# Kernel tuning notes

Hardware: AMD Instinct MI355X
Metric: run time of the kernel (lower is better)

The kernel has to match this reference:

```python
import jax, jax.numpy as jnp
import numpy as np

N = 100000   # nodes
E = 1600000  # edges (before self loops)
F = 64       # num_features
H = 64       # hidden_channels
C = 10       # num_classes
G = 128      # graphs in batch
NEG_SLOPE = 0.2


def setup_inputs() -> dict:
    key = jax.random.key(0)
    ks = jax.random.split(key, 16)
    x = jax.random.normal(ks[0], (N, F), dtype=jnp.float32)
    edge_index = jax.random.randint(ks[1], (2, E), 0, N, dtype=jnp.int64)
    batch = jnp.sort(jax.random.randint(ks[2], (N,), 0, G, dtype=jnp.int64))
    def glorot(k, shape):
        fan = shape[0] + shape[-1]
        return jax.random.uniform(k, shape, jnp.float32, -1.0, 1.0) * np.sqrt(6.0 / fan)
    return {
        "x": x, "edge_index": edge_index, "batch": batch,
        # GATConv 1 (F -> H)
        "W1": glorot(ks[3], (F, H)), "as1": glorot(ks[4], (H,)), "ad1": glorot(ks[5], (H,)), "b1": jnp.zeros((H,), jnp.float32),
        # GATConv 2 (H -> H)
        "W2": glorot(ks[6], (H, H)), "as2": glorot(ks[7], (H,)), "ad2": glorot(ks[8], (H,)), "b2": jnp.zeros((H,), jnp.float32),
        # MLP head
        "mw1": glorot(ks[9], (H, H)), "mb1": jnp.zeros((H,), jnp.float32),
        "mw2": glorot(ks[10], (H, C)), "mb2": jnp.zeros((C,), jnp.float32),
    }


def gat_conv(x, src, dst, W, a_s, a_d, b):
    # x: [N, Fin] -> h: [N, Fout]
    h = x @ W
    # per-node attention halves, gathered per edge (heads=1)
    al_s = h @ a_s   # [N]
    al_d = h @ a_d   # [N]
    e = jax.nn.leaky_relu(al_s[src] + al_d[dst], NEG_SLOPE)  # [E']
    # segment softmax over incoming edges of each destination node
    m = jax.ops.segment_max(e, dst, num_segments=N)
    ex = jnp.exp(e - m[dst])
    denom = jax.ops.segment_sum(ex, dst, num_segments=N)
    alpha = ex / denom[dst]                                   # [E']
    # weighted scatter-add of source features
    out = jax.ops.segment_sum(alpha[:, None] * h[src], dst, num_segments=N)
    return out + b


def reference(x, edge_index, batch, W1, as1, ad1, b1, W2, as2, ad2, b2, mw1, mb1, mw2, mb2):
    # add self loops (PyG GATConv default)
    loop = jnp.arange(N, dtype=edge_index.dtype)
    src = jnp.concatenate([edge_index[0], loop])
    dst = jnp.concatenate([edge_index[1], loop])

    h = gat_conv(x, src, dst, W1, as1, ad1, b1)
    h = jax.nn.elu(h)  # dropout p=0.5 is identity in eval mode
    h = gat_conv(h, src, dst, W2, as2, ad2, b2)
    h = jax.nn.elu(h)

    h = jax.nn.relu(h @ mw1 + mb1) @ mw2 + mb2   # MLP [N, C]
    return jax.ops.segment_sum(h, batch, num_segments=G)  # global_add_pool [G, C]
```

## Files before the change

kernel.cpp:

```cpp
#include <hip/hip_runtime.h>
#include <hip/hip_bf16.h>
#include <math.h>

#define SHIFT 20.0f
#define T_PER 16
#define TILE (256 * T_PER)
#define SEG_CAP 12288
#define BCAP 10240

typedef __bf16 bf16x8 __attribute__((ext_vector_type(8)));
typedef float  f32x4  __attribute__((ext_vector_type(4)));

__device__ __forceinline__ unsigned f2bf(float f) {
    unsigned u = __float_as_uint(f);
    return (u + 0x7fffu + ((u >> 16) & 1u)) >> 16;
}

__global__ void init_kernel(int* __restrict__ bcur, int K2,
                            float* __restrict__ Pz, int nPz)
{
    int t = threadIdx.x;
    if (t < K2) bcur[t * 16] = t * BCAP;
    for (int i = t; i < nPz; i += 256) Pz[i] = 0.f;
}

__global__ __launch_bounds__(256) void multisplit_kernel(
    const int* __restrict__ esrc, const int* __restrict__ edst,
    int* __restrict__ bcur, unsigned* __restrict__ pairbuf,
    int nE, int nN, int K2, int nTiles)
{
    __shared__ int lhist[256];
    __shared__ int lbase[256];
    int t = threadIdx.x;
    int tot = nE + nN;

    for (int tile = blockIdx.x; tile < nTiles; tile += gridDim.x) {
        int base = tile * TILE;
        if (t < K2) lhist[t] = 0;
        __syncthreads();

        unsigned pk[T_PER];
        int loc[T_PER];
        #pragma unroll
        for (int i = 0; i < T_PER; i++) {
            int e = base + t + i * 256;
            if (e < tot) {
                int s = (e < nE) ? esrc[e] : (e - nE);
                int d = (e < nE) ? edst[e] : (e - nE);
                int b = d >> 9;
                pk[i] = ((unsigned)s << 9) | (unsigned)(d & 511);
                int idx = atomicAdd(&lhist[b], 1);
                loc[i] = (b << 20) | idx;
            } else loc[i] = -1;
        }
        __syncthreads();
        if (t < K2) {
            int c = lhist[t];
            lbase[t] = (c > 0) ? atomicAdd(&bcur[t * 16], c) : 0;
        }
        __syncthreads();
        #pragma unroll
        for (int i = 0; i < T_PER; i++) {
            if (loc[i] >= 0)
                pairbuf[lbase[loc[i] >> 20] + (loc[i] & 0xFFFFF)] = pk[i];
        }
        __syncthreads();
    }
}

__global__ __launch_bounds__(256) void local_scatter_kernel(
    const unsigned* __restrict__ pairbuf, const int* __restrict__ bcur,
    int2* __restrict__ rp2, int* __restrict__ csr_src, int nN, int K2)
{
    __shared__ unsigned seg[SEG_CAP];
    __shared__ int lh[512];
    __shared__ int cur[512];
    __shared__ int psum[256];
    int b = blockIdx.x;
    int t = threadIdx.x;
    int d0 = b * 512;
    int nd = min(512, nN - d0);
    int lo = b * BCAP;
    int hi = bcur[b * 16];
    int len = hi - lo;
    bool inLds = (len <= SEG_CAP);

    lh[t] = 0; lh[t + 256] = 0;
    if (inLds)
        for (int j = t; j < len; j += 256) seg[j] = pairbuf[lo + j];
    __syncthreads();
    if (inLds) {
        for (int j = t; j < len; j += 256) atomicAdd(&lh[seg[j] & 511u], 1);
    } else {
        for (int j = lo + t; j < hi; j += 256)
            atomicAdd(&lh[pairbuf[j] & 511u], 1);
    }
    __syncthreads();

    int v0 = lh[2 * t], v1 = lh[2 * t + 1];
    int ps = v0 + v1;
    psum[t] = ps;
    __syncthreads();
    for (int off = 1; off < 256; off <<= 1) {
        int u = (t >= off) ? psum[t - off] : 0;
        __syncthreads();
        psum[t] += u;
        __syncthreads();
    }
    int e0 = lo + psum[t] - ps;
    int e1 = e0 + v0;
    cur[2 * t] = e0;
    cur[2 * t + 1] = e1;
    if (2 * t < nd)     rp2[d0 + 2 * t]     = make_int2(e0, v0);
    if (2 * t + 1 < nd) rp2[d0 + 2 * t + 1] = make_int2(e1, v1);
    __syncthreads();

    if (inLds) {
        for (int j = t; j < len; j += 256) {
            unsigned w = seg[j];
            int pos = atomicAdd(&cur[w & 511u], 1);
            csr_src[pos] = (int)(w >> 9);
        }
    } else {
        for (int j = lo + t; j < hi; j += 256) {
            unsigned w = pairbuf[j];
            int pos = atomicAdd(&cur[w & 511u], 1);
            csr_src[pos] = (int)(w >> 9);
        }
    }
}

__global__ void prep_kernel(const float* __restrict__ W1,
                            const float* __restrict__ as1, const float* __restrict__ ad1,
                            const float* __restrict__ W2,
                            const float* __restrict__ as2, const float* __restrict__ ad2,
                            const float* __restrict__ mw1,
                            uint4* __restrict__ Wf1, uint4* __restrict__ Wf2,
                            uint4* __restrict__ mwf)
{
    __shared__ float wasad[256];
    int t = threadIdx.x;
    {
        int k = t & 63;
        const float* W  = (t < 128) ? W1 : W2;
        const float* av = (t < 64) ? as1 : (t < 128) ? ad1 : (t < 192) ? as2 : ad2;
        float s = 0.f;
        for (int n = 0; n < 64; n++) s = fmaf(W[k * 64 + n], av[n], s);
        wasad[t] = s;
    }
    __syncthreads();

    for (int idx = t; idx < 1792; idx += 256) {
        const float* W; const float* wv; uint4* dst; int rem;
        if (idx < 640)       { rem = idx;        W = W1;  wv = &wasad[0];   dst = Wf1; }
        else if (idx < 1280) { rem = idx - 640;  W = W2;  wv = &wasad[128]; dst = Wf2; }
        else                 { rem = idx - 1280; W = mw1; wv = nullptr;     dst = mwf; }
        int pair = rem >> 6, l = rem & 63;
        int tt = pair >> 1, s = pair & 1;
        int kb = s * 32 + (l >> 4) * 8;
        unsigned d[4];
        if (tt < 4) {
            int n = tt * 16 + (l & 15);
            #pragma unroll
            for (int j = 0; j < 4; j++)
                d[j] = f2bf(W[(kb + 2 * j) * 64 + n]) |
                       (f2bf(W[(kb + 2 * j + 1) * 64 + n]) << 16);
        } else {
            int n0 = l & 15;
            #pragma unroll
            for (int j = 0; j < 4; j++) {
                float v0 = (n0 == 0) ? wv[kb + 2 * j]     : (n0 == 1) ? wv[64 + kb + 2 * j]     : 0.f;
                float v1 = (n0 == 0) ? wv[kb + 2 * j + 1] : (n0 == 1) ? wv[64 + kb + 2 * j + 1] : 0.f;
                d[j] = f2bf(v0) | (f2bf(v1) << 16);
            }
        }
        dst[pair * 64 + l] = make_uint4(d[0], d[1], d[2], d[3]);
    }
}

__global__ __launch_bounds__(256) void gemm_att_mfma(
    const void* __restrict__ Xv, int x_is_bf16,
    const uint4* __restrict__ Wf,
    __hip_bfloat16* __restrict__ Hout,
    float* __restrict__ als, float* __restrict__ ald, int nN)
{
    __shared__ __align__(16) unsigned char lds[256 * 144];
    int t = threadIdx.x, lane = t & 63, wv = t >> 6;
    int b0 = blockIdx.x * 256;

    uint4 wf[10];
    #pragma unroll
    for (int p = 0; p < 10; p++) wf[p] = Wf[p * 64 + lane];

    if (x_is_bf16) {
        const uint4* X4 = (const uint4*)Xv;
        int limit = nN * 8;
        #pragma unroll
        for (int k = 0; k < 8; k++) {
            int dst = t + k * 256;
            int idx = b0 * 8 + dst;
            if (idx < limit) {
                int r = dst >> 3, c = dst & 7;
                *(uint4*)(lds + r * 144 + c * 16) = X4[idx];
            }
        }
    } else {
        const float4* Xf = (const float4*)Xv;
        int limit = nN * 16;
        #pragma unroll
        for (int k = 0; k < 16; k++) {
            int dst = t + k * 256;
            int idx = b0 * 16 + dst;
            if (idx < limit) {
                float4 v = Xf[idx];
                uint2 r2;
                r2.x = f2bf(v.x) | (f2bf(v.y) << 16);
                r2.y = f2bf(v.z) | (f2bf(v.w) << 16);
                int r = dst >> 4, c = dst & 15;
                *(uint2*)(lds + r * 144 + c * 8) = r2;
            }
        }
    }
    __syncthreads();

    f32x4 acc[4][5] = {};
    int rbase = wv * 64;
    #pragma unroll
    for (int s = 0; s < 2; s++) {
        #pragma unroll
        for (int rf = 0; rf < 4; rf++) {
            const uint4 av = *(const uint4*)(lds + (rbase + rf * 16 + (lane & 15)) * 144
                                                 + s * 64 + (lane >> 4) * 16);
            bf16x8 a = __builtin_bit_cast(bf16x8, av);
            #pragma unroll
            for (int tt = 0; tt < 5; tt++) {
                bf16x8 b = __builtin_bit_cast(bf16x8, wf[tt * 2 + s]);
                acc[rf][tt] = __builtin_amdgcn_mfma_f32_16x16x32_bf16(a, b, acc[rf][tt], 0, 0, 0);
            }
        }
    }

    int q = lane >> 4, c = lane & 15;
    #pragma unroll
    for (int rf = 0; rf < 4; rf++) {
        #pragma unroll
        for (int r = 0; r < 4; r++) {
            int n = b0 + rbase + rf * 16 + q * 4 + r;
            if (n < nN) {
                #pragma unroll
                for (int tt = 0; tt < 4; tt++)
                    Hout[(size_t)n * 64 + tt * 16 + c] = __float2bfloat16(acc[rf][tt][r]);
                if (c == 0)      als[n] = acc[rf][4][r];
                else if (c == 1) ald[n] = acc[rf][4][r];
            }
        }
    }
}

__global__ __launch_bounds__(256) void pull_kernel(
    const int* __restrict__ csr_src, const int2* __restrict__ rp2,
    const unsigned* __restrict__ Hu,
    const float* __restrict__ als, const float* __restrict__ ald,
    const float* __restrict__ bias,
    __hip_bfloat162* __restrict__ out2, int nN)
{
    int lane = threadIdx.x & 63;
    int half = lane >> 5;
    int fl = lane & 31;
    int wid  = (blockIdx.x * blockDim.x + threadIdx.x) >> 6;
    int nw   = (gridDim.x * blockDim.x) >> 6;
    float2 bl2 = ((const float2*)bias)[fl];

    for (int d = wid; d < nN; d += nw) {
        int2 rp = rp2[d];
        int s0 = rp.x, s1 = rp.x + rp.y;
        float aldd = ald[d];
        float aclo = 0.f, achi = 0.f, den = 0.f;

        for (int base = s0; base < s1; base += 64) {
            int j = base + lane;
            bool v = (j < s1);
            int sl = v ? csr_src[j] : 0;
            float ex = 0.f;
            if (v) {
                float sc = als[sl] + aldd;
                sc = (sc > 0.f) ? sc : 0.2f * sc;
                ex = __expf(sc - SHIFT);
            }
            float es = ex;
            #pragma unroll
            for (int off = 32; off > 0; off >>= 1) es += __shfl_xor(es, off);
            den += es;

            int m = min(64, s1 - base);
            int i2 = 0;
            for (; i2 + 3 < m; i2 += 4) {
                int iA = i2 + half, iB = i2 + 2 + half;
                int sA = __shfl(sl, iA), sB = __shfl(sl, iB);
                float eA = __shfl(ex, iA), eB = __shfl(ex, iB);
                unsigned dA = Hu[(size_t)sA * 32 + fl];
                unsigned dB = Hu[(size_t)sB * 32 + fl];
                aclo = fmaf(eA, __uint_as_float(dA << 16), aclo);
                achi = fmaf(eA, __uint_as_float(dA & 0xffff0000u), achi);
                aclo = fmaf(eB, __uint_as_float(dB << 16), aclo);
                achi = fmaf(eB, __uint_as_float(dB & 0xffff0000u), achi);
            }
            for (; i2 < m; i2 += 2) {
                int idx = i2 + half;
                int s = __shfl(sl, idx);
                float e = (idx < m) ? __shfl(ex, idx) : 0.f;
                unsigned dd = Hu[(size_t)s * 32 + fl];
                aclo = fmaf(e, __uint_as_float(dd << 16), aclo);
                achi = fmaf(e, __uint_as_float(dd & 0xffff0000u), achi);
            }
        }
        aclo += __shfl_xor(aclo, 32);
        achi += __shfl_xor(achi, 32);
        float v0 = aclo / den + bl2.x;
        float v1 = achi / den + bl2.y;
        v0 = (v0 > 0.f) ? v0 : expm1f(v0);
        v1 = (v1 > 0.f) ? v1 : expm1f(v1);
        if (half == 0) {
            __hip_bfloat162 pk;
            pk.x = __float2bfloat16(v0);
            pk.y = __float2bfloat16(v1);
            out2[(size_t)d * 32 + fl] = pk;
        }
    }
}

__global__ __launch_bounds__(256) void mlp_pool_mfma(
    const uint4* __restrict__ Hin,
    const uint4* __restrict__ mwf, const float* __restrict__ mb1,
    const int* __restrict__ batch,
    float* __restrict__ P, float* __restrict__ Pcnt, int nN)
{
    __shared__ __align__(16) unsigned char lds[256 * 144];
    int t = threadIdx.x, lane = t & 63, wv = t >> 6;
    int b0 = blockIdx.x * 256;

    uint4 wf[8];
    #pragma unroll
    for (int p = 0; p < 8; p++) wf[p] = mwf[p * 64 + lane];

    int limit = nN * 8;
    #pragma unroll
    for (int k = 0; k < 8; k++) {
        int dst = t + k * 256;
        int idx = b0 * 8 + dst;
        if (idx < limit) {
            int r = dst >> 3, c = dst & 7;
            *(uint4*)(lds + r * 144 + c * 16) = Hin[idx];
        }
    }
    __syncthreads();

    f32x4 acc[4][4] = {};
    int rbase = wv * 64;
    #pragma unroll
    for (int s = 0; s < 2; s++) {
        #pragma unroll
        for (int rf = 0; rf < 4; rf++) {
            const uint4 av = *(const uint4*)(lds + (rbase + rf * 16 + (lane & 15)) * 144
                                                 + s * 64 + (lane >> 4) * 16);
            bf16x8 a = __builtin_bit_cast(bf16x8, av);
            #pragma unroll
            for (int tt = 0; tt < 4; tt++) {
                bf16x8 b = __builtin_bit_cast(bf16x8, wf[tt * 2 + s]);
                acc[rf][tt] = __builtin_amdgcn_mfma_f32_16x16x32_bf16(a, b, acc[rf][tt], 0, 0, 0);
            }
        }
    }

    int q = lane >> 4, c = lane & 15;
    float bl0 = mb1[c], bl1 = mb1[16 + c], bl2 = mb1[32 + c], bl3 = mb1[48 + c];
    float r0 = 0.f, r1 = 0.f, r2 = 0.f, r3 = 0.f, ccnt = 0.f;
    int gcur = -1;
    #pragma unroll
    for (int rf = 0; rf < 4; rf++) {
        #pragma unroll
        for (int r = 0; r < 4; r++) {
            int n = b0 + rbase + rf * 16 + q * 4 + r;
            if (n < nN) {
                int g = batch[n];
                if (g != gcur) {
                    if (gcur >= 0) {
                        atomicAdd(&P[(size_t)gcur * 64 + c],      r0);
                        atomicAdd(&P[(size_t)gcur * 64 + 16 + c], r1);
                        atomicAdd(&P[(size_t)gcur * 64 + 32 + c], r2);
                        atomicAdd(&P[(size_t)gcur * 64 + 48 + c], r3);
                        if (c == 0) atomicAdd(&Pcnt[gcur], ccnt);
                    }
                    gcur = g; r0 = r1 = r2 = r3 = 0.f; ccnt = 0.f;
                }
                r0 += fmaxf(acc[rf][0][r] + bl0, 0.f);
                r1 += fmaxf(acc[rf][1][r] + bl1, 0.f);
                r2 += fmaxf(acc[rf][2][r] + bl2, 0.f);
                r3 += fmaxf(acc[rf][3][r] + bl3, 0.f);
                ccnt += 1.f;
            }
        }
    }
    if (gcur >= 0) {
        atomicAdd(&P[(size_t)gcur * 64 + c],      r0);
        atomicAdd(&P[(size_t)gcur * 64 + 16 + c], r1);
        atomicAdd(&P[(size_t)gcur * 64 + 32 + c], r2);
        atomicAdd(&P[(size_t)gcur * 64 + 48 + c], r3);
        if (c == 0) atomicAdd(&Pcnt[gcur], ccnt);
    }
}

__global__ void head_out_kernel(const float* __restrict__ P,
                                const float* __restrict__ Pcnt,
                                const float* __restrict__ mw2,
                                const float* __restrict__ mb2,
                                float* __restrict__ out, int nOut)
{
    int t = blockIdx.x * blockDim.x + threadIdx.x;
    if (t >= nOut) return;
    int g = t / 10, j = t % 10;
    float s = mb2[j] * Pcnt[g];
    const float* pr = P + (size_t)g * 64;
    #pragma unroll
    for (int k = 0; k < 64; k++) s = fmaf(pr[k], mw2[k * 10 + j], s);
    out[t] = s;
}

extern "C" void kernel_launch(void* const* d_in, const int* in_sizes, int n_in,
                              void* d_out, int out_size, void* d_ws, size_t ws_size,
                              hipStream_t stream)
{
    const float* x   = (const float*)d_in[0];
    const int*  eidx = (const int*)d_in[1];
    const int* batch = (const int*)d_in[2];
    const float* W1  = (const float*)d_in[3];
    const float* as1 = (const float*)d_in[4];
    const float* ad1 = (const float*)d_in[5];
    const float* b1  = (const float*)d_in[6];
    const float* W2  = (const float*)d_in[7];
    const float* as2 = (const float*)d_in[8];
    const float* ad2 = (const float*)d_in[9];
    const float* b2  = (const float*)d_in[10];
    const float* mw1 = (const float*)d_in[11];
    const float* mb1 = (const float*)d_in[12];
    const float* mw2 = (const float*)d_in[13];
    const float* mb2 = (const float*)d_in[14];
    float* out = (float*)d_out;

    int nN = in_sizes[0] / 64;
    int nE = in_sizes[1] / 2;
    int tot = nE + nN;
    int K2 = (nN + 511) >> 9;
    int G  = out_size / 10;
    const int* esrc = eidx;
    const int* edst = eidx + nE;

    float* ws = (float*)d_ws;
    size_t NF = (size_t)nN * 64;
    size_t capTot = (size_t)K2 * BCAP;
    float* bufA   = ws;
    float* bufB   = ws + NF;
    float* als    = ws + 2 * NF;
    float* ald    = als + nN;
    int2* rp2     = (int2*)(ald + nN);
    int* csr_src  = (int*)(rp2 + nN);
    int* bcur     = csr_src + capTot;
    float* P      = (float*)(bcur + K2 * 16 + 15);
    float* Pcnt   = P + (size_t)G * 64;
    uintptr_t wb  = ((uintptr_t)(Pcnt + G) + 255) & ~(uintptr_t)255;
    uint4* Wf1    = (uint4*)wb;
    uint4* Wf2    = Wf1 + 640;
    uint4* mwf    = Wf2 + 640;
    unsigned* pairbuf = (unsigned*)bufA;
    __hip_bfloat16* hbf = (__hip_bfloat16*)bufB;

    dim3 blk(256);
    int nTiles = (tot + TILE - 1) / TILE;
    int nT256 = (nN + 255) / 256;

    init_kernel<<<1, blk, 0, stream>>>(bcur, K2, P, G * 64 + G);
    multisplit_kernel<<<nTiles, blk, 0, stream>>>(esrc, edst, bcur, pairbuf,
                                                  nE, nN, K2, nTiles);
    local_scatter_kernel<<<K2, blk, 0, stream>>>(pairbuf, bcur, rp2,
                                                 csr_src, nN, K2);

    prep_kernel<<<1, blk, 0, stream>>>(W1, as1, ad1, W2, as2, ad2, mw1,
                                       Wf1, Wf2, mwf);

    gemm_att_mfma<<<nT256, blk, 0, stream>>>(x, 0, Wf1, hbf, als, ald, nN);
    pull_kernel<<<2048, blk, 0, stream>>>(csr_src, rp2, (const unsigned*)hbf,
                                          als, ald, b1,
                                          (__hip_bfloat162*)bufA, nN);
    gemm_att_mfma<<<nT256, blk, 0, stream>>>(bufA, 1, Wf2, hbf, als, ald, nN);
    pull_kernel<<<2048, blk, 0, stream>>>(csr_src, rp2, (const unsigned*)hbf,
                                          als, ald, b2,
                                          (__hip_bfloat162*)bufA, nN);

    mlp_pool_mfma<<<nT256, blk, 0, stream>>>((const uint4*)bufA, mwf, mb1,
                                             batch, P, Pcnt, nN);
    head_out_kernel<<<(out_size + 255) / 256, blk, 0, stream>>>(P, Pcnt, mw2,
                                                                mb2, out, out_size);
}
```

Measured before the change: 303.7 us.

## Widen pull gathers to 4 edges per pass, merge setup kernels, enlarge scatter blocks

The pull kernel now has each lane gather 8 bytes (4 bf16 features) so that a wave processes 4 edges per iteration instead of 2. It then reduces across the quarter-waves with two xor shuffles and multiplies by the reciprocal of the denominator instead of dividing. The init and weight-prep kernels are merged into one 2-block launch to save a launch. The local scatter uses 1024-thread blocks with a 512-wide scan, and the multisplit tile is halved for more blocks. These trade per-lane work and extra shuffles against fewer gather iterations and more parallelism in the CSR build.

```diff
diff --git a/kernel.cpp b/kernel.cpp
--- a/kernel.cpp
+++ b/kernel.cpp
@@ -3,10 +3,11 @@
 #include <math.h>
 
 #define SHIFT 20.0f
-#define T_PER 16
+#define T_PER 8
 #define TILE (256 * T_PER)
 #define SEG_CAP 12288
 #define BCAP 10240
+#define LS_T 1024
 
 typedef __bf16 bf16x8 __attribute__((ext_vector_type(8)));
 typedef float  f32x4  __attribute__((ext_vector_type(4)));
@@ -16,130 +17,23 @@
     return (u + 0x7fffu + ((u >> 16) & 1u)) >> 16;
 }
 
-__global__ void init_kernel(int* __restrict__ bcur, int K2,
-                            float* __restrict__ Pz, int nPz)
+__global__ void setup_kernel(int* __restrict__ bcur, int K2,
+                             float* __restrict__ Pz, int nPz,
+                             const float* __restrict__ W1,
+                             const float* __restrict__ as1, const float* __restrict__ ad1,
+                             const float* __restrict__ W2,
+                             const float* __restrict__ as2, const float* __restrict__ ad2,
+                             const float* __restrict__ mw1,
+                             uint4* __restrict__ Wf1, uint4* __restrict__ Wf2,
+                             uint4* __restrict__ mwf)
 {
     int t = threadIdx.x;
-    if (t < K2) bcur[t * 16] = t * BCAP;
-    for (int i = t; i < nPz; i += 256) Pz[i] = 0.f;
-}
-
-__global__ __launch_bounds__(256) void multisplit_kernel(
-    const int* __restrict__ esrc, const int* __restrict__ edst,
-    int* __restrict__ bcur, unsigned* __restrict__ pairbuf,
-    int nE, int nN, int K2, int nTiles)
-{
-    __shared__ int lhist[256];
-    __shared__ int lbase[256];
-    int t = threadIdx.x;
-    int tot = nE + nN;
-
-    for (int tile = blockIdx.x; tile < nTiles; tile += gridDim.x) {
-        int base = tile * TILE;
-        if (t < K2) lhist[t] = 0;
-        __syncthreads();
-
-        unsigned pk[T_PER];
-        int loc[T_PER];
-        #pragma unroll
-        for (int i = 0; i < T_PER; i++) {
-            int e = base + t + i * 256;
-            if (e < tot) {
-                int s = (e < nE) ? esrc[e] : (e - nE);
-                int d = (e < nE) ? edst[e] : (e - nE);
-                int b = d >> 9;
-                pk[i] = ((unsigned)s << 9) | (unsigned)(d & 511);
-                int idx = atomicAdd(&lhist[b], 1);
-                loc[i] = (b << 20) | idx;
-            } else loc[i] = -1;
-        }
-        __syncthreads();
-        if (t < K2) {
-            int c = lhist[t];
-            lbase[t] = (c > 0) ? atomicAdd(&bcur[t * 16], c) : 0;
-        }
-        __syncthreads();
-        #pragma unroll
-        for (int i = 0; i < T_PER; i++) {
-            if (loc[i] >= 0)
-                pairbuf[lbase[loc[i] >> 20] + (loc[i] & 0xFFFFF)] = pk[i];
-        }
-        __syncthreads();
-    }
-}
-
-__global__ __launch_bounds__(256) void local_scatter_kernel(
-    const unsigned* __restrict__ pairbuf, const int* __restrict__ bcur,
-    int2* __restrict__ rp2, int* __restrict__ csr_src, int nN, int K2)
-{
-    __shared__ unsigned seg[SEG_CAP];
-    __shared__ int lh[512];
-    __shared__ int cur[512];
-    __shared__ int psum[256];
-    int b = blockIdx.x;
-    int t = threadIdx.x;
-    int d0 = b * 512;
-    int nd = min(512, nN - d0);
-    int lo = b * BCAP;
-    int hi = bcur[b * 16];
-    int len = hi - lo;
-    bool inLds = (len <= SEG_CAP);
-
-    lh[t] = 0; lh[t + 256] = 0;
-    if (inLds)
-        for (int j = t; j < len; j += 256) seg[j] = pairbuf[lo + j];
-    __syncthreads();
-    if (inLds) {
-        for (int j = t; j < len; j += 256) atomicAdd(&lh[seg[j] & 511u], 1);
-    } else {
-        for (int j = lo + t; j < hi; j += 256)
-            atomicAdd(&lh[pairbuf[j] & 511u], 1);
-    }
-    __syncthreads();
-
-    int v0 = lh[2 * t], v1 = lh[2 * t + 1];
-    int ps = v0 + v1;
-    psum[t] = ps;
-    __syncthreads();
-    for (int off = 1; off < 256; off <<= 1) {
-        int u = (t >= off) ? psum[t - off] : 0;
-        __syncthreads();
-        psum[t] += u;
-        __syncthreads();
-    }
-    int e0 = lo + psum[t] - ps;
-    int e1 = e0 + v0;
-    cur[2 * t] = e0;
-    cur[2 * t + 1] = e1;
-    if (2 * t < nd)     rp2[d0 + 2 * t]     = make_int2(e0, v0);
-    if (2 * t + 1 < nd) rp2[d0 + 2 * t + 1] = make_int2(e1, v1);
-    __syncthreads();
-
-    if (inLds) {
-        for (int j = t; j < len; j += 256) {
-            unsigned w = seg[j];
-            int pos = atomicAdd(&cur[w & 511u], 1);
-            csr_src[pos] = (int)(w >> 9);
-        }
-    } else {
-        for (int j = lo + t; j < hi; j += 256) {
-            unsigned w = pairbuf[j];
-            int pos = atomicAdd(&cur[w & 511u], 1);
-            csr_src[pos] = (int)(w >> 9);
-        }
-    }
-}
-
-__global__ void prep_kernel(const float* __restrict__ W1,
-                            const float* __restrict__ as1, const float* __restrict__ ad1,
-                            const float* __restrict__ W2,
-                            const float* __restrict__ as2, const float* __restrict__ ad2,
-                            const float* __restrict__ mw1,
-                            uint4* __restrict__ Wf1, uint4* __restrict__ Wf2,
-                            uint4* __restrict__ mwf)
-{
+    if (blockIdx.x == 0) {
+        if (t < K2) bcur[t * 16] = t * BCAP;
+        for (int i = t; i < nPz; i += 256) Pz[i] = 0.f;
+        return;
+    }
     __shared__ float wasad[256];
-    int t = threadIdx.x;
     {
         int k = t & 63;
         const float* W  = (t < 128) ? W1 : W2;
@@ -178,6 +72,110 @@
     }
 }
 
+__global__ __launch_bounds__(256) void multisplit_kernel(
+    const int* __restrict__ esrc, const int* __restrict__ edst,
+    int* __restrict__ bcur, unsigned* __restrict__ pairbuf,
+    int nE, int nN, int K2, int nTiles)
+{
+    __shared__ int lhist[256];
+    __shared__ int lbase[256];
+    int t = threadIdx.x;
+    int tot = nE + nN;
+
+    for (int tile = blockIdx.x; tile < nTiles; tile += gridDim.x) {
+        int base = tile * TILE;
+        if (t < K2) lhist[t] = 0;
+        __syncthreads();
+
+        unsigned pk[T_PER];
+        int loc[T_PER];
+        #pragma unroll
+        for (int i = 0; i < T_PER; i++) {
+            int e = base + t + i * 256;
+            if (e < tot) {
+                int s = (e < nE) ? esrc[e] : (e - nE);
+                int d = (e < nE) ? edst[e] : (e - nE);
+                int b = d >> 9;
+                pk[i] = ((unsigned)s << 9) | (unsigned)(d & 511);
+                int idx = atomicAdd(&lhist[b], 1);
+                loc[i] = (b << 20) | idx;
+            } else loc[i] = -1;
+        }
+        __syncthreads();
+        if (t < K2) {
+            int c = lhist[t];
+            lbase[t] = (c > 0) ? atomicAdd(&bcur[t * 16], c) : 0;
+        }
+        __syncthreads();
+        #pragma unroll
+        for (int i = 0; i < T_PER; i++) {
+            if (loc[i] >= 0)
+                pairbuf[lbase[loc[i] >> 20] + (loc[i] & 0xFFFFF)] = pk[i];
+        }
+        __syncthreads();
+    }
+}
+
+__global__ __launch_bounds__(LS_T) void local_scatter_kernel(
+    const unsigned* __restrict__ pairbuf, const int* __restrict__ bcur,
+    int2* __restrict__ rp2, int* __restrict__ csr_src, int nN, int K2)
+{
+    __shared__ unsigned seg[SEG_CAP];
+    __shared__ int lh[512];
+    __shared__ int cur[512];
+    __shared__ int psum[512];
+    int b = blockIdx.x;
+    int t = threadIdx.x;
+    int d0 = b * 512;
+    int nd = min(512, nN - d0);
+    int lo = b * BCAP;
+    int hi = bcur[b * 16];
+    int len = hi - lo;
+    bool inLds = (len <= SEG_CAP);
+
+    if (t < 512) lh[t] = 0;
+    if (inLds)
+        for (int j = t; j < len; j += LS_T) seg[j] = pairbuf[lo + j];
+    __syncthreads();
+    if (inLds) {
+        for (int j = t; j < len; j += LS_T) atomicAdd(&lh[seg[j] & 511u], 1);
+    } else {
+        for (int j = lo + t; j < hi; j += LS_T)
+            atomicAdd(&lh[pairbuf[j] & 511u], 1);
+    }
+    __syncthreads();
+
+    int v = (t < 512) ? lh[t] : 0;
+    if (t < 512) psum[t] = v;
+    __syncthreads();
+    for (int off = 1; off < 512; off <<= 1) {
+        int u = (t < 512 && t >= off) ? psum[t - off] : 0;
+        __syncthreads();
+        if (t < 512) psum[t] += u;
+        __syncthreads();
+    }
+    if (t < 512) {
+        int e0 = lo + psum[t] - v;
+        cur[t] = e0;
+        if (t < nd) rp2[d0 + t] = make_int2(e0, v);
+    }
+    __syncthreads();
+
+    if (inLds) {
+        for (int j = t; j < len; j += LS_T) {
+            unsigned w = seg[j];
+            int pos = atomicAdd(&cur[w & 511u], 1);
+            csr_src[pos] = (int)(w >> 9);
+        }
+    } else {
+        for (int j = lo + t; j < hi; j += LS_T) {
+            unsigned w = pairbuf[j];
+            int pos = atomicAdd(&cur[w & 511u], 1);
+            csr_src[pos] = (int)(w >> 9);
+        }
+    }
+}
+
 __global__ __launch_bounds__(256) void gemm_att_mfma(
     const void* __restrict__ Xv, int x_is_bf16,
     const uint4* __restrict__ Wf,
@@ -259,23 +257,23 @@
 
 __global__ __launch_bounds__(256) void pull_kernel(
     const int* __restrict__ csr_src, const int2* __restrict__ rp2,
-    const unsigned* __restrict__ Hu,
+    const uint2* __restrict__ Hu2,
     const float* __restrict__ als, const float* __restrict__ ald,
     const float* __restrict__ bias,
-    __hip_bfloat162* __restrict__ out2, int nN)
+    uint2* __restrict__ out2, int nN)
 {
     int lane = threadIdx.x & 63;
-    int half = lane >> 5;
-    int fl = lane & 31;
+    int eq = lane >> 4;
+    int fq = lane & 15;
     int wid  = (blockIdx.x * blockDim.x + threadIdx.x) >> 6;
     int nw   = (gridDim.x * blockDim.x) >> 6;
-    float2 bl2 = ((const float2*)bias)[fl];
+    float4 bl = ((const float4*)bias)[fq];
 
     for (int d = wid; d < nN; d += nw) {
         int2 rp = rp2[d];
         int s0 = rp.x, s1 = rp.x + rp.y;
         float aldd = ald[d];
-        float aclo = 0.f, achi = 0.f, den = 0.f;
+        float a0 = 0.f, a1 = 0.f, a2 = 0.f, a3 = 0.f, den = 0.f;
 
         for (int base = s0; base < s1; base += 64) {
             int j = base + lane;
@@ -293,38 +291,35 @@
             den += es;
 
             int m = min(64, s1 - base);
-            int i2 = 0;
-            for (; i2 + 3 < m; i2 += 4) {
-                int iA = i2 + half, iB = i2 + 2 + half;
-                int sA = __shfl(sl, iA), sB = __shfl(sl, iB);
-                float eA = __shfl(ex, iA), eB = __shfl(ex, iB);
-                unsigned dA = Hu[(size_t)sA * 32 + fl];
-                unsigned dB = Hu[(size_t)sB * 32 + fl];
-                aclo = fmaf(eA, __uint_as_float(dA << 16), aclo);
-                achi = fmaf(eA, __uint_as_float(dA & 0xffff0000u), achi);
-                aclo = fmaf(eB, __uint_as_float(dB << 16), aclo);
-                achi = fmaf(eB, __uint_as_float(dB & 0xffff0000u), achi);
-            }
-            for (; i2 < m; i2 += 2) {
-                int idx = i2 + half;
+            for (int i2 = 0; i2 < m; i2 += 4) {
+                int idx = i2 + eq;
                 int s = __shfl(sl, idx);
-                float e = (idx < m) ? __shfl(ex, idx) : 0.f;
-                unsigned dd = Hu[(size_t)s * 32 + fl];
-                aclo = fmaf(e, __uint_as_float(dd << 16), aclo);
-                achi = fmaf(e, __uint_as_float(dd & 0xffff0000u), achi);
-            }
-        }
-        aclo += __shfl_xor(aclo, 32);
-        achi += __shfl_xor(achi, 32);
-        float v0 = aclo / den + bl2.x;
-        float v1 = achi / den + bl2.y;
-        v0 = (v0 > 0.f) ? v0 : expm1f(v0);
-        v1 = (v1 > 0.f) ? v1 : expm1f(v1);
-        if (half == 0) {
-            __hip_bfloat162 pk;
-            pk.x = __float2bfloat16(v0);
-            pk.y = __float2bfloat16(v1);
-            out2[(size_t)d * 32 + fl] = pk;
+                float e = __shfl(ex, idx);
+                uint2 dd = Hu2[(unsigned)s * 16 + fq];
+                a0 = fmaf(e, __uint_as_float(dd.x << 16), a0);
+                a1 = fmaf(e, __uint_as_float(dd.x & 0xffff0000u), a1);
+                a2 = fmaf(e, __uint_as_float(dd.y << 16), a2);
+                a3 = fmaf(e, __uint_as_float(dd.y & 0xffff0000u), a3);
+            }
+        }
+        a0 += __shfl_xor(a0, 16); a0 += __shfl_xor(a0, 32);
+        a1 += __shfl_xor(a1, 16); a1 += __shfl_xor(a1, 32);
+        a2 += __shfl_xor(a2, 16); a2 += __shfl_xor(a2, 32);
+        a3 += __shfl_xor(a3, 16); a3 += __shfl_xor(a3, 32);
+        if (eq == 0) {
+            float r = 1.f / den;
+            float v0 = a0 * r + bl.x;
+            float v1 = a1 * r + bl.y;
+            float v2 = a2 * r + bl.z;
+            float v3 = a3 * r + bl.w;
+            v0 = (v0 > 0.f) ? v0 : expm1f(v0);
+            v1 = (v1 > 0.f) ? v1 : expm1f(v1);
+            v2 = (v2 > 0.f) ? v2 : expm1f(v2);
+            v3 = (v3 > 0.f) ? v3 : expm1f(v3);
+            uint2 pk;
+            pk.x = f2bf(v0) | (f2bf(v1) << 16);
+            pk.y = f2bf(v2) | (f2bf(v3) << 16);
+            out2[(size_t)d * 16 + fq] = pk;
         }
     }
 }
@@ -478,23 +473,20 @@
     int nTiles = (tot + TILE - 1) / TILE;
     int nT256 = (nN + 255) / 256;
 
-    init_kernel<<<1, blk, 0, stream>>>(bcur, K2, P, G * 64 + G);
+    setup_kernel<<<2, blk, 0, stream>>>(bcur, K2, P, G * 64 + G,
+                                        W1, as1, ad1, W2, as2, ad2, mw1,
+                                        Wf1, Wf2, mwf);
     multisplit_kernel<<<nTiles, blk, 0, stream>>>(esrc, edst, bcur, pairbuf,
                                                   nE, nN, K2, nTiles);
-    local_scatter_kernel<<<K2, blk, 0, stream>>>(pairbuf, bcur, rp2,
-                                                 csr_src, nN, K2);
-
-    prep_kernel<<<1, blk, 0, stream>>>(W1, as1, ad1, W2, as2, ad2, mw1,
-                                       Wf1, Wf2, mwf);
+    local_scatter_kernel<<<K2, dim3(LS_T), 0, stream>>>(pairbuf, bcur, rp2,
+                                                        csr_src, nN, K2);
 
     gemm_att_mfma<<<nT256, blk, 0, stream>>>(x, 0, Wf1, hbf, als, ald, nN);
-    pull_kernel<<<2048, blk, 0, stream>>>(csr_src, rp2, (const unsigned*)hbf,
-                                          als, ald, b1,
-                                          (__hip_bfloat162*)bufA, nN);
+    pull_kernel<<<2048, blk, 0, stream>>>(csr_src, rp2, (const uint2*)hbf,
+                                          als, ald, b1, (uint2*)bufA, nN);
     gemm_att_mfma<<<nT256, blk, 0, stream>>>(bufA, 1, Wf2, hbf, als, ald, nN);
-    pull_kernel<<<2048, blk, 0, stream>>>(csr_src, rp2, (const unsigned*)hbf,
-                                          als, ald, b2,
-                                          (__hip_bfloat162*)bufA, nN);
+    pull_kernel<<<2048, blk, 0, stream>>>(csr_src, rp2, (const uint2*)hbf,
+                                          als, ald, b2, (uint2*)bufA, nN);
 
     mlp_pool_mfma<<<nT256, blk, 0, stream>>>((const uint4*)bufA, mwf, mb1,
                                              batch, P, Pcnt, nN);
```

After: 307.6 us. About the same (+1.3%).
